# Kernel optimization log

Measured on AMD Instinct MI355X. Metric: run time of the kernel, lower is better.

The kernel has to match this reference:

```python
import math
import jax, jax.numpy as jnp
import numpy as np

NUM_HEADS = 16


def setup_inputs() -> dict:
    key = jax.random.key(0)
    ks = jax.random.split(key, 5)
    B, S, H = 2, 2048, 1024
    hidden_states = jax.random.normal(ks[0], (B, S, H), dtype=jnp.float32)
    # causal lower-triangular float mask [1, 1, S, S], as the module expects
    ltor_mask = jnp.tril(jnp.ones((S, S), dtype=jnp.float32))[None, None, :, :]
    # weights stored pre-transposed: y = x @ W + b (equivalent to torch Linear)
    W_qkv = jax.random.normal(ks[1], (H, 3 * H), dtype=jnp.float32) * (1.0 / math.sqrt(H))
    b_qkv = jnp.zeros((3 * H,), dtype=jnp.float32)
    W_dense = jax.random.normal(ks[2], (H, H), dtype=jnp.float32) * (1.0 / math.sqrt(H))
    b_dense = jnp.zeros((H,), dtype=jnp.float32)
    return {
        "hidden_states": hidden_states,
        "ltor_mask": ltor_mask,
        "W_qkv": W_qkv,
        "b_qkv": b_qkv,
        "W_dense": W_dense,
        "b_dense": b_dense,
    }


def reference(hidden_states, ltor_mask, W_qkv, b_qkv, W_dense, b_dense):
    B, S, H = hidden_states.shape
    nh = NUM_HEADS
    hd = H // nh

    # fused QKV projection: [B, S, 3H] -> split -> [B, nh, S, hd]
    qkv = hidden_states @ W_qkv + b_qkv
    q, k, v = jnp.split(qkv, 3, axis=-1)

    def to_heads(x):
        return x.reshape(B, S, nh, hd).transpose(0, 2, 1, 3)

    q, k, v = to_heads(q), to_heads(k), to_heads(v)

    # scaled dot-product scores [B, nh, S, S]
    scores = jnp.einsum("bhqd,bhkd->bhqk", q, k) / math.sqrt(hd)
    # mul/sub causal masking, exactly as the torch module does
    scores = scores * ltor_mask - 10000.0 * (1.0 - ltor_mask)
    probs = jax.nn.softmax(scores, axis=-1)
    # attention dropout omitted (eval mode / p=0.0)

    ctx = jnp.einsum("bhqk,bhkd->bhqd", probs, v)
    ctx = ctx.transpose(0, 2, 1, 3).reshape(B, S, H)

    out = ctx @ W_dense + b_dense
    # output dropout omitted (eval mode / p=0.0)
    return out
```

## Files before the change

kernel.cpp:

```cpp
#include <hip/hip_runtime.h>
#include <math.h>

#define BATCH 2
#define SEQ   2048
#define HID   1024
#define NHEAD 16
#define HDIM  64
#define MTOT  (BATCH * SEQ)
#define QKVN  (3 * HID)
#define HBUF  ((size_t)BATCH * NHEAD * SEQ * HDIM)

typedef _Float16 f16x8 __attribute__((ext_vector_type(8)));
typedef _Float16 f16x4 __attribute__((ext_vector_type(4)));
typedef float    f32x4 __attribute__((ext_vector_type(4)));

#define MFMA16(a, b, c) __builtin_amdgcn_mfma_f32_16x16x32_f16((a), (b), (c), 0, 0, 0)

#define GLDS16(gp, lp) __builtin_amdgcn_global_load_lds( \
    (const __attribute__((address_space(1))) void*)(gp), \
    (__attribute__((address_space(3))) void*)(lp), 16, 0, 0)

#if __has_builtin(__builtin_amdgcn_exp2f)
#define EXP2F(x) __builtin_amdgcn_exp2f(x)
#else
#define EXP2F(x) exp2f(x)
#endif

#define SCALE2 0.18033688011f
#define MASK2  -14426.950408f
#define BIAS2  -4.0f

__global__ __launch_bounds__(256) void prep_kernel(
    const float* __restrict__ hs, const float* __restrict__ Wqkv,
    const float* __restrict__ Wd, _Float16* __restrict__ A_h,
    _Float16* __restrict__ outQ, _Float16* __restrict__ outD)
{
    __shared__ _Float16 T[32][36];
    const int gid = blockIdx.x;
    const int tid = threadIdx.x;
    if (gid < 2048) {
        const int ci = gid * 256 + tid;
        const int m = ci >> 7, cc = ci & 127;
        const float* src = hs + (size_t)m * 1024 + cc * 8;
        f16x8 o;
#pragma unroll
        for (int j = 0; j < 8; ++j) o[j] = (_Float16)src[j];
        *(f16x8*)(A_h + (size_t)m * 1024 + cc * 8) = o;
        return;
    }
    const int tb = gid - 2048;
    const int bx = tb & 127, k0 = (tb >> 7) * 32;
    const float* in;
    _Float16* out;
    int N, n0;
    bool isQ;
    if (bx < 96) { in = Wqkv; out = outQ; N = QKVN; n0 = bx * 32; isQ = true; }
    else         { in = Wd;   out = outD; N = HID;  n0 = (bx - 96) * 32; isQ = false; }
    {
        const int r = tid >> 3, c4 = (tid & 7) * 4;
        float4 v = *(const float4*)(in + (size_t)(k0 + r) * N + n0 + c4);
        T[r][c4 + 0] = (_Float16)v.x;
        T[r][c4 + 1] = (_Float16)v.y;
        T[r][c4 + 2] = (_Float16)v.z;
        T[r][c4 + 3] = (_Float16)v.w;
    }
    __syncthreads();
    {
        const int nn = tid >> 3, k4 = (tid & 7) * 4;
        const int n = n0 + nn;
        f16x4 o;
        o[0] = T[k4 + 0][nn]; o[1] = T[k4 + 1][nn];
        o[2] = T[k4 + 2][nn]; o[3] = T[k4 + 3][nn];
        if (isQ) {
            *(f16x4*)(out + (size_t)n * 1024 + k0 + k4) = o;
        } else {
            const int pos = ((k4 >> 3) ^ (n & 3)), half = (k4 >> 2) & 1;
            *(f16x4*)(out + (size_t)n * 1024 + k0 + pos * 8 + half * 4) = o;
        }
    }
}

__global__ __launch_bounds__(512, 1) void qkv_gemm8(
    const _Float16* __restrict__ A, const _Float16* __restrict__ Bt,
    const float* __restrict__ bias, _Float16* __restrict__ base)
{
    __shared__ _Float16 SA[2][16384];
    __shared__ _Float16 SB[2][12288];
    const int tid = threadIdx.x;
    const int w = tid >> 6, l = tid & 63;
    const int a = l & 15, q4 = l >> 4, a7 = a & 7;
    const int xc = blockIdx.x & 7, loc = blockIdx.x >> 3;
    const int bx = (xc & 3) * 4 + (loc & 3);
    const int by = (xc >> 2) * 8 + (loc >> 2);
    const int m0 = by * 256, n0 = bx * 192;
    const int wm = (w >> 2) * 128, wn = (w & 3) * 48;

    const int csw = (((tid & 7) ^ ((tid >> 3) & 7)) << 3);
    const _Float16* gA0 = A  + (size_t)(m0 + (tid >> 3)) * 1024 + csw;
    const _Float16* gB0 = Bt + (size_t)(n0 + (tid >> 3)) * 1024 + csw;

    auto stage = [&](int kt, int sl) {
        const size_t ko = (size_t)kt * 64;
#pragma unroll
        for (int u = 0; u < 4; ++u)
            GLDS16(gA0 + (size_t)(u * 64) * 1024 + ko, &SA[sl][0] + u * 4096 + tid * 8);
#pragma unroll
        for (int u = 0; u < 3; ++u)
            GLDS16(gB0 + (size_t)(u * 64) * 1024 + ko, &SB[sl][0] + u * 4096 + tid * 8);
    };

    stage(0, 0); stage(1, 1);
    asm volatile("s_waitcnt vmcnt(7)" ::: "memory");
    __builtin_amdgcn_sched_barrier(0);
    __builtin_amdgcn_s_barrier();
    __builtin_amdgcn_sched_barrier(0);

    f32x4 acc[8][3];
#pragma unroll
    for (int i = 0; i < 8; ++i)
#pragma unroll
        for (int j = 0; j < 3; ++j) acc[i][j] = (f32x4){0.f, 0.f, 0.f, 0.f};

#define FRG(SP, row_, ks_) \
    (*(const f16x8*)&(SP)[(row_) * 64 + ((((ks_) * 4 + q4) ^ a7) << 3)])

    f16x8 aL[4][2], aH[4][2], bf[3][2];
    {
#pragma unroll
        for (int i = 0; i < 4; ++i) {
            aL[i][0] = FRG(SA[0], wm + i * 16 + a, 0);
            aL[i][1] = FRG(SA[0], wm + i * 16 + a, 1);
        }
#pragma unroll
        for (int j = 0; j < 2; ++j) {
            bf[j][0] = FRG(SB[0], wn + j * 16 + a, 0);
            bf[j][1] = FRG(SB[0], wn + j * 16 + a, 1);
        }
    }

    for (int t = 0; t < 16; ++t) {
        const int sl = t & 1, nsl = sl ^ 1;
        const _Float16* sA = &SA[sl][0];
        const _Float16* sB = &SB[sl][0];

        if (t >= 1 && t <= 14) stage(t + 1, nsl);

        __builtin_amdgcn_s_setprio(1);
#pragma unroll
        for (int i = 0; i < 4; ++i)
#pragma unroll
            for (int j = 0; j < 2; ++j) {
                acc[i][j] = MFMA16(aL[i][0], bf[j][0], acc[i][j]);
                acc[i][j] = MFMA16(aL[i][1], bf[j][1], acc[i][j]);
            }
        __builtin_amdgcn_s_setprio(0);

        bf[2][0] = FRG(sB, wn + 32 + a, 0);
        bf[2][1] = FRG(sB, wn + 32 + a, 1);
        __builtin_amdgcn_s_setprio(1);
#pragma unroll
        for (int i = 0; i < 4; ++i) {
            acc[i][2] = MFMA16(aL[i][0], bf[2][0], acc[i][2]);
            acc[i][2] = MFMA16(aL[i][1], bf[2][1], acc[i][2]);
        }
        __builtin_amdgcn_s_setprio(0);

#pragma unroll
        for (int i = 0; i < 4; ++i) {
            aH[i][0] = FRG(sA, wm + 64 + i * 16 + a, 0);
            aH[i][1] = FRG(sA, wm + 64 + i * 16 + a, 1);
        }
        __builtin_amdgcn_s_setprio(1);
#pragma unroll
        for (int i = 0; i < 4; ++i)
#pragma unroll
            for (int j = 0; j < 3; ++j) {
                acc[i + 4][j] = MFMA16(aH[i][0], bf[j][0], acc[i + 4][j]);
                acc[i + 4][j] = MFMA16(aH[i][1], bf[j][1], acc[i + 4][j]);
            }
        __builtin_amdgcn_s_setprio(0);

        if (t < 15) {
            asm volatile("s_waitcnt vmcnt(0)" ::: "memory");
            __builtin_amdgcn_sched_barrier(0);
            __builtin_amdgcn_s_barrier();
            __builtin_amdgcn_sched_barrier(0);
            const _Float16* nA = &SA[nsl][0];
            const _Float16* nB = &SB[nsl][0];
#pragma unroll
            for (int i = 0; i < 4; ++i) {
                aL[i][0] = FRG(nA, wm + i * 16 + a, 0);
                aL[i][1] = FRG(nA, wm + i * 16 + a, 1);
            }
#pragma unroll
            for (int j = 0; j < 2; ++j) {
                bf[j][0] = FRG(nB, wn + j * 16 + a, 0);
                bf[j][1] = FRG(nB, wn + j * 16 + a, 1);
            }
        }
    }
#undef FRG

#pragma unroll
    for (int j = 0; j < 3; ++j) {
        const int n = n0 + wn + 16 * j + a;
        const float bv = bias[n];
        const int tq = n >> 10, h = (n >> 6) & 15, d = n & 63;
#pragma unroll
        for (int i = 0; i < 8; ++i) {
            const int mb = m0 + wm + 16 * i + q4 * 4;
            const int bb = mb >> 11, sb = mb & 2047;
            if (tq == 2) {
                f16x4 ov;
#pragma unroll
                for (int r = 0; r < 4; ++r) ov[r] = (_Float16)(acc[i][j][r] + bv);
                const size_t off =
                    ((size_t)((bb * 16 + h) * 64 + d)) * 2048
                    + (sb & ~63)
                    + ((((sb >> 3) & 7) ^ (d & 7)) << 3) + (sb & 7);
                *(f16x4*)(base + 3 * HBUF + off) = ov;
            } else if (tq == 1) {
#pragma unroll
                for (int r = 0; r < 4; ++r) {
                    const int s = sb + r;
                    const _Float16 val = (_Float16)(acc[i][j][r] + bv);
                    const int dk = ((((d >> 3) ^ (s & 7)) & 7) << 3) | (d & 7);
                    base[HBUF + ((size_t)(bb * 16 + h) * 2048 + s) * 64 + dk] = val;
                }
            } else {
#pragma unroll
                for (int r = 0; r < 4; ++r) {
                    const _Float16 val = (_Float16)(acc[i][j][r] + bv);
                    base[((size_t)(bb * 16 + h) * 2048 + sb + r) * 64 + d] = val;
                }
            }
        }
    }
}

template<int EPI, int TM>
__global__ __launch_bounds__(256) void mfma_gemm(
    const _Float16* __restrict__ A, const _Float16* __restrict__ Bt,
    const float* __restrict__ bias, void* __restrict__ Cout,
    int M, int N, int K)
{
    __shared__ _Float16 As[TM * 32];
    __shared__ _Float16 Bs[128 * 32];
    constexpr int TI = TM / 32;
    constexpr int AR = TM / 4;

    const int tid = threadIdx.x;
    const int w = tid >> 6, l = tid & 63;
    const int a = l & 15, q4 = l >> 4;
    const int m0 = blockIdx.y * TM, n0 = blockIdx.x * 128;
    const int wm = (w >> 1) * (TM / 2), wn = (w & 1) * 64;

    f32x4 acc[TI][4];
#pragma unroll
    for (int i = 0; i < TI; ++i)
#pragma unroll
        for (int j = 0; j < 4; ++j) acc[i][j] = (f32x4){0.f, 0.f, 0.f, 0.f};

    const _Float16* gA = A + (size_t)(m0 + w * AR + (l >> 2)) * K + (l & 3) * 8;
    const _Float16* gB = Bt + (size_t)(n0 + w * 32 + (l >> 2)) * K + (l & 3) * 8;
    _Float16* sA = As + w * AR * 32;
    _Float16* sB = Bs + w * 1024;

    for (int k0 = 0; k0 < K; k0 += 32) {
#pragma unroll
        for (int u = 0; u < TM / 64; ++u)
            GLDS16(gA + (size_t)u * 16 * K + k0, sA + u * 512);
        GLDS16(gB + k0,          sB);
        GLDS16(gB + 16 * K + k0, sB + 512);
        __syncthreads();

        f16x8 af[TI], bf[4];
        const int pa = (q4 ^ (a & 3)) << 3;
#pragma unroll
        for (int i = 0; i < TI; ++i)
            af[i] = *(const f16x8*)&As[(wm + 16 * i + a) * 32 + pa];
#pragma unroll
        for (int j = 0; j < 4; ++j)
            bf[j] = *(const f16x8*)&Bs[(wn + 16 * j + a) * 32 + pa];
#pragma unroll
        for (int i = 0; i < TI; ++i)
#pragma unroll
            for (int j = 0; j < 4; ++j)
                acc[i][j] = MFMA16(af[i], bf[j], acc[i][j]);
        __syncthreads();
    }

    {
        float* C = (float*)Cout;
#pragma unroll
        for (int j = 0; j < 4; ++j) {
            const int n = n0 + wn + 16 * j + a;
            const float bv = bias[n];
#pragma unroll
            for (int i = 0; i < TI; ++i)
#pragma unroll
                for (int r = 0; r < 4; ++r) {
                    const int m = m0 + wm + 16 * i + q4 * 4 + r;
                    C[(size_t)m * N + n] = acc[i][j][r] + bv;
                }
        }
    }
}

__global__ __launch_bounds__(256, 2) void attn_mfma(
    const _Float16* __restrict__ qb, const _Float16* __restrict__ kb,
    const _Float16* __restrict__ vtb, _Float16* __restrict__ ctx)
{
    __shared__ _Float16 Ks[2][64 * 64];
    __shared__ _Float16 VT[2][64 * 64];
    __shared__ _Float16 Ps[4][16 * 64];

    const int bid = blockIdx.x;
    const int jj = bid >> 3;
    const int bhIdx = (bid & 7) * 4 + (jj >> 4);
    const int p = jj & 15;
    const int b = bhIdx >> 4, h = bhIdx & 15;
    const int tid = threadIdx.x;
    const int w = tid >> 6, l = tid & 63;
    const int a = l & 15, q4 = l >> 4, a7 = a & 7;
    const size_t bh  = ((size_t)b * NHEAD + h) * SEQ;
    const size_t bhd = ((size_t)b * NHEAD + h) * 64;

    const int qHi = (31 - p) * 64 + w * 16;
    const int qLo = p * 64 + w * 16;
    const int ntiles = 32 - p;

    f16x8 qfh[2], qfl[2];
    {
        const _Float16* qp = qb + (bh + qHi + a) * 64;
        qfh[0] = *(const f16x8*)(qp + q4 * 8);
        qfh[1] = *(const f16x8*)(qp + 32 + q4 * 8);
        const _Float16* ql = qb + (bh + qLo + a) * 64;
        qfl[0] = *(const f16x8*)(ql + q4 * 8);
        qfl[1] = *(const f16x8*)(ql + 32 + q4 * 8);
    }

    f32x4 Oh[4], Ol[4];
#pragma unroll
    for (int c = 0; c < 4; ++c) {
        Oh[c] = (f32x4){0.f, 0.f, 0.f, 0.f};
        Ol[c] = (f32x4){0.f, 0.f, 0.f, 0.f};
    }
    float lh = 0.f, ll = 0.f;

    const _Float16* kg = kb + (bh + w * 16) * 64 + l * 8;
    const int vrow = w * 16 + (l >> 3);
    const _Float16* vg = vtb + (bhd + vrow) * 2048 + (l & 7) * 8;
    _Float16* pbuf = &Ps[w][0];
    const int p0 = (q4 ^ a7) << 3;

    auto stage = [&](int t, int buf) {
        _Float16* ksl = &Ks[buf][0] + w * 1024 + l * 8;
        const _Float16* kt = kg + (size_t)t * 4096;
        GLDS16(kt,       ksl);
        GLDS16(kt + 512, ksl + 512);
        _Float16* vtl = &VT[buf][0] + vrow * 64 + (l & 7) * 8;
        GLDS16(vg + t * 64,            vtl);
        GLDS16(vg + t * 64 + 8 * 2048, vtl + 512);
    };

    stage(0, 0);

    for (int t = 0; t < ntiles; ++t) {
        __syncthreads();
        if (t + 1 < ntiles) stage(t + 1, (t + 1) & 1);

        const _Float16* ksb  = &Ks[t & 1][0];
        const _Float16* vbuf = &VT[t & 1][0];
        const int kt0 = t * 64;
        const bool doLo = (t <= p);

        f32x4 sh[4], sl[4];
        __builtin_amdgcn_s_setprio(1);
#pragma unroll
        for (int n0 = 0; n0 < 4; ++n0) {
            f16x8 kf0 = *(const f16x8*)&ksb[(n0 * 16 + a) * 64 + p0];
            f16x8 kf1 = *(const f16x8*)&ksb[(n0 * 16 + a) * 64 + (p0 ^ 32)];
            f32x4 c = (f32x4){0.f, 0.f, 0.f, 0.f};
            c = MFMA16(kf0, qfh[0], c);
            c = MFMA16(kf1, qfh[1], c);
            sh[n0] = c;
            if (doLo) {
                f32x4 d = (f32x4){0.f, 0.f, 0.f, 0.f};
                d = MFMA16(kf0, qfl[0], d);
                d = MFMA16(kf1, qfl[1], d);
                sl[n0] = d;
            }
        }
        __builtin_amdgcn_s_setprio(0);

        auto half_step = [&](f32x4 st[4], float& lrun, f32x4* O,
                             const bool maskT, const int qbase) {
            if (maskT) {
#pragma unroll
                for (int n0 = 0; n0 < 4; ++n0)
#pragma unroll
                    for (int r = 0; r < 4; ++r) {
                        const int kgl = kt0 + n0 * 16 + q4 * 4 + r;
                        st[n0][r] = (kgl > qbase + a) ? MASK2
                                                      : fmaf(st[n0][r], SCALE2, BIAS2);
                    }
            } else {
#pragma unroll
                for (int n0 = 0; n0 < 4; ++n0)
#pragma unroll
                    for (int r = 0; r < 4; ++r)
                        st[n0][r] = fmaf(st[n0][r], SCALE2, BIAS2);
            }
            float ls = 0.f;
#pragma unroll
            for (int n0 = 0; n0 < 4; ++n0)
#pragma unroll
                for (int r = 0; r < 4; ++r) {
                    const float pe = EXP2F(st[n0][r]);
                    st[n0][r] = pe;
                    ls += pe;
                }
            lrun += ls;
#pragma unroll
            for (int n0 = 0; n0 < 4; ++n0) {
                f16x4 pk;
#pragma unroll
                for (int r = 0; r < 4; ++r) pk[r] = (_Float16)st[n0][r];
                const int pos = (2 * n0 + (q4 >> 1)) ^ a7;
                *(f16x4*)&pbuf[a * 64 + pos * 8 + ((q4 & 1) << 2)] = pk;
            }
            f16x8 pf0 = *(const f16x8*)&pbuf[a * 64 + p0];
            f16x8 pf1 = *(const f16x8*)&pbuf[a * 64 + (p0 ^ 32)];
            __builtin_amdgcn_s_setprio(1);
#pragma unroll
            for (int c = 0; c < 4; ++c) {
                f16x8 vf0 = *(const f16x8*)&vbuf[(c * 16 + a) * 64 + p0];
                f16x8 vf1 = *(const f16x8*)&vbuf[(c * 16 + a) * 64 + (p0 ^ 32)];
                O[c] = MFMA16(vf0, pf0, O[c]);
                O[c] = MFMA16(vf1, pf1, O[c]);
            }
            __builtin_amdgcn_s_setprio(0);
        };

        half_step(sh, lh, Oh, t == 31 - p, qHi);
        if (doLo) half_step(sl, ll, Ol, t == p, qLo);
    }

    auto finish = [&](float lrun, const f32x4* O, const int qbase) {
        float lt = lrun;
        lt += __shfl_xor(lt, 16);
        lt += __shfl_xor(lt, 32);
        const float inv = 1.0f / lt;
        const size_t row = (size_t)b * SEQ + qbase + a;
#pragma unroll
        for (int c = 0; c < 4; ++c) {
            const int d0 = c * 16 + q4 * 4;
            const int kcol = h * 64 + (d0 & ~31)
                           + ((((d0 >> 3) & 3) ^ (a & 3)) << 3) + (d0 & 7);
            f16x4 ov;
#pragma unroll
            for (int r = 0; r < 4; ++r) ov[r] = (_Float16)(O[c][r] * inv);
            *(f16x4*)(ctx + row * HID + kcol) = ov;
        }
    };
    finish(lh, Oh, qHi);
    finish(ll, Ol, qLo);
}

extern "C" void kernel_launch(void* const* d_in, const int* in_sizes, int n_in,
                              void* d_out, int out_size, void* d_ws, size_t ws_size,
                              hipStream_t stream) {
    const float* hs   = (const float*)d_in[0];
    const float* Wqkv = (const float*)d_in[2];
    const float* bqkv = (const float*)d_in[3];
    const float* Wd   = (const float*)d_in[4];
    const float* bd   = (const float*)d_in[5];

    _Float16* A_h   = (_Float16*)d_ws;
    _Float16* WqkvT = A_h + (size_t)MTOT * HID;
    _Float16* WdT   = WqkvT + (size_t)QKVN * HID;
    _Float16* qbuf  = WdT + (size_t)HID * HID;
    _Float16* ctxb  = qbuf + 4 * HBUF;

    prep_kernel<<<6144, 256, 0, stream>>>(hs, Wqkv, Wd, A_h, WqkvT, WdT);

    qkv_gemm8<<<256, 512, 0, stream>>>(A_h, WqkvT, bqkv, qbuf);

    attn_mfma<<<512, 256, 0, stream>>>(
        qbuf, qbuf + HBUF, qbuf + 3 * HBUF, ctxb);

    mfma_gemm<1, 64><<<dim3(HID / 128, MTOT / 64), 256, 0, stream>>>(
        ctxb, WdT, bd, d_out, MTOT, HID, HID);
}
```

Measured before the change: 185.4 us.

## Split attention KV tiles across two wave groups and merge partial outputs

Doubles the attention block to 512 threads. Two groups of four waves each process alternating KV tiles for the same query rows, using separate double-buffered K/V shared memory, then combine their partial O and row sums through shared memory before normalising. This works because the softmax uses a fixed offset instead of a running max, so partial sums can simply be added. It aims to shorten the serial KV loop per block and raise wave-level parallelism on the MI355X's 256 CUs, at the cost of more shared memory, an extra reduction step, and possible occupancy limits with launch_bounds(512,2).

Measured after the change: 190.4 us. 1.03x slower.

```diff
diff --git a/kernel.cpp b/kernel.cpp
--- a/kernel.cpp
+++ b/kernel.cpp
@@ -307,13 +307,13 @@
     }
 }
 
-__global__ __launch_bounds__(256, 2) void attn_mfma(
+__global__ __launch_bounds__(512, 2) void attn_mfma(
     const _Float16* __restrict__ qb, const _Float16* __restrict__ kb,
     const _Float16* __restrict__ vtb, _Float16* __restrict__ ctx)
 {
-    __shared__ _Float16 Ks[2][64 * 64];
-    __shared__ _Float16 VT[2][64 * 64];
-    __shared__ _Float16 Ps[4][16 * 64];
+    __shared__ _Float16 Ks[2][2][64 * 64];
+    __shared__ _Float16 VT[2][2][64 * 64];
+    __shared__ _Float16 Ps[8][16 * 64];
 
     const int bid = blockIdx.x;
     const int jj = bid >> 3;
@@ -322,13 +322,15 @@
     const int b = bhIdx >> 4, h = bhIdx & 15;
     const int tid = threadIdx.x;
     const int w = tid >> 6, l = tid & 63;
+    const int sgrp = w >> 2, w4 = w & 3;
     const int a = l & 15, q4 = l >> 4, a7 = a & 7;
     const size_t bh  = ((size_t)b * NHEAD + h) * SEQ;
     const size_t bhd = ((size_t)b * NHEAD + h) * 64;
 
-    const int qHi = (31 - p) * 64 + w * 16;
-    const int qLo = p * 64 + w * 16;
+    const int qHi = (31 - p) * 64 + w4 * 16;
+    const int qLo = p * 64 + w4 * 16;
     const int ntiles = 32 - p;
+    const int NIT = (ntiles + 1) >> 1;
 
     f16x8 qfh[2], qfl[2];
     {
@@ -348,124 +350,156 @@
     }
     float lh = 0.f, ll = 0.f;
 
-    const _Float16* kg = kb + (bh + w * 16) * 64 + l * 8;
-    const int vrow = w * 16 + (l >> 3);
+    const _Float16* kg = kb + (bh + w4 * 16) * 64 + l * 8;
+    const int vrow = w4 * 16 + (l >> 3);
     const _Float16* vg = vtb + (bhd + vrow) * 2048 + (l & 7) * 8;
     _Float16* pbuf = &Ps[w][0];
     const int p0 = (q4 ^ a7) << 3;
 
     auto stage = [&](int t, int buf) {
-        _Float16* ksl = &Ks[buf][0] + w * 1024 + l * 8;
+        _Float16* ksl = &Ks[sgrp][buf][0] + w4 * 1024 + l * 8;
         const _Float16* kt = kg + (size_t)t * 4096;
         GLDS16(kt,       ksl);
         GLDS16(kt + 512, ksl + 512);
-        _Float16* vtl = &VT[buf][0] + vrow * 64 + (l & 7) * 8;
+        _Float16* vtl = &VT[sgrp][buf][0] + vrow * 64 + (l & 7) * 8;
         GLDS16(vg + t * 64,            vtl);
         GLDS16(vg + t * 64 + 8 * 2048, vtl + 512);
     };
 
-    stage(0, 0);
-
-    for (int t = 0; t < ntiles; ++t) {
+    stage(sgrp, 0);
+
+    for (int it = 0; it < NIT; ++it) {
         __syncthreads();
-        if (t + 1 < ntiles) stage(t + 1, (t + 1) & 1);
-
-        const _Float16* ksb  = &Ks[t & 1][0];
-        const _Float16* vbuf = &VT[t & 1][0];
-        const int kt0 = t * 64;
-        const bool doLo = (t <= p);
-
-        f32x4 sh[4], sl[4];
-        __builtin_amdgcn_s_setprio(1);
-#pragma unroll
-        for (int n0 = 0; n0 < 4; ++n0) {
-            f16x8 kf0 = *(const f16x8*)&ksb[(n0 * 16 + a) * 64 + p0];
-            f16x8 kf1 = *(const f16x8*)&ksb[(n0 * 16 + a) * 64 + (p0 ^ 32)];
-            f32x4 c = (f32x4){0.f, 0.f, 0.f, 0.f};
-            c = MFMA16(kf0, qfh[0], c);
-            c = MFMA16(kf1, qfh[1], c);
-            sh[n0] = c;
-            if (doLo) {
-                f32x4 d = (f32x4){0.f, 0.f, 0.f, 0.f};
-                d = MFMA16(kf0, qfl[0], d);
-                d = MFMA16(kf1, qfl[1], d);
-                sl[n0] = d;
-            }
-        }
-        __builtin_amdgcn_s_setprio(0);
-
-        auto half_step = [&](f32x4 st[4], float& lrun, f32x4* O,
-                             const bool maskT, const int qbase) {
-            if (maskT) {
+        const int t = sgrp + 2 * it;
+        const int buf = it & 1;
+        if (t + 2 < ntiles) stage(t + 2, buf ^ 1);
+        if (t < ntiles) {
+            const _Float16* ksb  = &Ks[sgrp][buf][0];
+            const _Float16* vbuf = &VT[sgrp][buf][0];
+            const int kt0 = t * 64;
+            const bool doLo = (t <= p);
+
+            f32x4 sh[4], sl[4];
+            __builtin_amdgcn_s_setprio(1);
+#pragma unroll
+            for (int n0 = 0; n0 < 4; ++n0) {
+                f16x8 kf0 = *(const f16x8*)&ksb[(n0 * 16 + a) * 64 + p0];
+                f16x8 kf1 = *(const f16x8*)&ksb[(n0 * 16 + a) * 64 + (p0 ^ 32)];
+                f32x4 c = (f32x4){0.f, 0.f, 0.f, 0.f};
+                c = MFMA16(kf0, qfh[0], c);
+                c = MFMA16(kf1, qfh[1], c);
+                sh[n0] = c;
+                if (doLo) {
+                    f32x4 d = (f32x4){0.f, 0.f, 0.f, 0.f};
+                    d = MFMA16(kf0, qfl[0], d);
+                    d = MFMA16(kf1, qfl[1], d);
+                    sl[n0] = d;
+                }
+            }
+            __builtin_amdgcn_s_setprio(0);
+
+            auto half_step = [&](f32x4 st[4], float& lrun, f32x4* O,
+                                 const bool maskT, const int qbase) {
+                if (maskT) {
+#pragma unroll
+                    for (int n0 = 0; n0 < 4; ++n0)
+#pragma unroll
+                        for (int r = 0; r < 4; ++r) {
+                            const int kgl = kt0 + n0 * 16 + q4 * 4 + r;
+                            st[n0][r] = (kgl > qbase + a) ? MASK2
+                                                          : fmaf(st[n0][r], SCALE2, BIAS2);
+                        }
+                } else {
+#pragma unroll
+                    for (int n0 = 0; n0 < 4; ++n0)
+#pragma unroll
+                        for (int r = 0; r < 4; ++r)
+                            st[n0][r] = fmaf(st[n0][r], SCALE2, BIAS2);
+                }
+                float ls = 0.f;
 #pragma unroll
                 for (int n0 = 0; n0 < 4; ++n0)
 #pragma unroll
                     for (int r = 0; r < 4; ++r) {
-                        const int kgl = kt0 + n0 * 16 + q4 * 4 + r;
-                        st[n0][r] = (kgl > qbase + a) ? MASK2
-                                                      : fmaf(st[n0][r], SCALE2, BIAS2);
+                        const float pe = EXP2F(st[n0][r]);
+                        st[n0][r] = pe;
+                        ls += pe;
                     }
-            } else {
-#pragma unroll
-                for (int n0 = 0; n0 < 4; ++n0)
-#pragma unroll
-                    for (int r = 0; r < 4; ++r)
-                        st[n0][r] = fmaf(st[n0][r], SCALE2, BIAS2);
-            }
-            float ls = 0.f;
-#pragma unroll
-            for (int n0 = 0; n0 < 4; ++n0)
-#pragma unroll
-                for (int r = 0; r < 4; ++r) {
-                    const float pe = EXP2F(st[n0][r]);
-                    st[n0][r] = pe;
-                    ls += pe;
-                }
-            lrun += ls;
-#pragma unroll
-            for (int n0 = 0; n0 < 4; ++n0) {
-                f16x4 pk;
-#pragma unroll
-                for (int r = 0; r < 4; ++r) pk[r] = (_Float16)st[n0][r];
-                const int pos = (2 * n0 + (q4 >> 1)) ^ a7;
-                *(f16x4*)&pbuf[a * 64 + pos * 8 + ((q4 & 1) << 2)] = pk;
-            }
-            f16x8 pf0 = *(const f16x8*)&pbuf[a * 64 + p0];
-            f16x8 pf1 = *(const f16x8*)&pbuf[a * 64 + (p0 ^ 32)];
-            __builtin_amdgcn_s_setprio(1);
+                lrun += ls;
+#pragma unroll
+                for (int n0 = 0; n0 < 4; ++n0) {
+                    f16x4 pk;
+#pragma unroll
+                    for (int r = 0; r < 4; ++r) pk[r] = (_Float16)st[n0][r];
+                    const int pos = (2 * n0 + (q4 >> 1)) ^ a7;
+                    *(f16x4*)&pbuf[a * 64 + pos * 8 + ((q4 & 1) << 2)] = pk;
+                }
+                f16x8 pf0 = *(const f16x8*)&pbuf[a * 64 + p0];
+                f16x8 pf1 = *(const f16x8*)&pbuf[a * 64 + (p0 ^ 32)];
+                __builtin_amdgcn_s_setprio(1);
+#pragma unroll
+                for (int c = 0; c < 4; ++c) {
+                    f16x8 vf0 = *(const f16x8*)&vbuf[(c * 16 + a) * 64 + p0];
+                    f16x8 vf1 = *(const f16x8*)&vbuf[(c * 16 + a) * 64 + (p0 ^ 32)];
+                    O[c] = MFMA16(vf0, pf0, O[c]);
+                    O[c] = MFMA16(vf1, pf1, O[c]);
+                }
+                __builtin_amdgcn_s_setprio(0);
+            };
+
+            half_step(sh, lh, Oh, t == 31 - p, qHi);
+            if (doLo) half_step(sl, ll, Ol, t == p, qLo);
+        }
+    }
+
+    __syncthreads();
+    float* cO = (float*)&Ks[0][0][0];
+    float* cL = (float*)&VT[0][0][0];
+    if (sgrp == 1) {
+        const int cbase = w4 * 2048;
+#pragma unroll
+        for (int c = 0; c < 4; ++c)
+#pragma unroll
+            for (int r = 0; r < 4; ++r) {
+                cO[cbase + (c * 4 + r) * 64 + l]        = Oh[c][r];
+                cO[cbase + (16 + c * 4 + r) * 64 + l]   = Ol[c][r];
+            }
+        cL[w4 * 128 + l]      = lh;
+        cL[w4 * 128 + 64 + l] = ll;
+    }
+    __syncthreads();
+    if (sgrp == 0) {
+        const int cbase = w4 * 2048;
+#pragma unroll
+        for (int c = 0; c < 4; ++c)
+#pragma unroll
+            for (int r = 0; r < 4; ++r) {
+                Oh[c][r] += cO[cbase + (c * 4 + r) * 64 + l];
+                Ol[c][r] += cO[cbase + (16 + c * 4 + r) * 64 + l];
+            }
+        lh += cL[w4 * 128 + l];
+        ll += cL[w4 * 128 + 64 + l];
+
+        auto finish = [&](float lrun, const f32x4* O, const int qbase) {
+            float lt = lrun;
+            lt += __shfl_xor(lt, 16);
+            lt += __shfl_xor(lt, 32);
+            const float inv = 1.0f / lt;
+            const size_t row = (size_t)b * SEQ + qbase + a;
 #pragma unroll
             for (int c = 0; c < 4; ++c) {
-                f16x8 vf0 = *(const f16x8*)&vbuf[(c * 16 + a) * 64 + p0];
-                f16x8 vf1 = *(const f16x8*)&vbuf[(c * 16 + a) * 64 + (p0 ^ 32)];
-                O[c] = MFMA16(vf0, pf0, O[c]);
-                O[c] = MFMA16(vf1, pf1, O[c]);
-            }
-            __builtin_amdgcn_s_setprio(0);
+                const int d0 = c * 16 + q4 * 4;
+                const int kcol = h * 64 + (d0 & ~31)
+                               + ((((d0 >> 3) & 3) ^ (a & 3)) << 3) + (d0 & 7);
+                f16x4 ov;
+#pragma unroll
+                for (int r = 0; r < 4; ++r) ov[r] = (_Float16)(O[c][r] * inv);
+                *(f16x4*)(ctx + row * HID + kcol) = ov;
+            }
         };
-
-        half_step(sh, lh, Oh, t == 31 - p, qHi);
-        if (doLo) half_step(sl, ll, Ol, t == p, qLo);
-    }
-
-    auto finish = [&](float lrun, const f32x4* O, const int qbase) {
-        float lt = lrun;
-        lt += __shfl_xor(lt, 16);
-        lt += __shfl_xor(lt, 32);
-        const float inv = 1.0f / lt;
-        const size_t row = (size_t)b * SEQ + qbase + a;
-#pragma unroll
-        for (int c = 0; c < 4; ++c) {
-            const int d0 = c * 16 + q4 * 4;
-            const int kcol = h * 64 + (d0 & ~31)
-                           + ((((d0 >> 3) & 3) ^ (a & 3)) << 3) + (d0 & 7);
-            f16x4 ov;
-#pragma unroll
-            for (int r = 0; r < 4; ++r) ov[r] = (_Float16)(O[c][r] * inv);
-            *(f16x4*)(ctx + row * HID + kcol) = ov;
-        }
-    };
-    finish(lh, Oh, qHi);
-    finish(ll, Ol, qLo);
+        finish(lh, Oh, qHi);
+        finish(ll, Ol, qLo);
+    }
 }
 
 extern "C" void kernel_launch(void* const* d_in, const int* in_sizes, int n_in,
@@ -487,7 +521,7 @@
 
     qkv_gemm8<<<256, 512, 0, stream>>>(A_h, WqkvT, bqkv, qbuf);
 
-    attn_mfma<<<512, 256, 0, stream>>>(
+    attn_mfma<<<512, 512, 0, stream>>>(
         qbuf, qbuf + HBUF, qbuf + 3 * HBUF, ctxb);
 
     mfma_gemm<1, 64><<<dim3(HID / 128, MTOT / 64), 256, 0, stream>>>(
```

## Load K/V attention fragments directly from global memory instead of LDS staging

Applied to the files above, without the earlier changes.

The attention kernel no longer double-buffers K and V tiles in shared memory through async global-to-LDS copies with a barrier each iteration. Each wave now loads its own K and V MFMA fragments straight from global memory into registers. To make that possible, the QKV projection epilogue now writes K and transposed V in plain unswizzled layouts. The intent is to remove per-tile barriers and LDS traffic, at the cost of four-fold redundant global/L2 loads per block and less latency hiding. The occupancy hint of 2 blocks per CU is also dropped from launch_bounds.

Result: slower. 260.8 us (+40.7%).

```diff
diff --git a/kernel.cpp b/kernel.cpp
--- a/kernel.cpp
+++ b/kernel.cpp
@@ -214,24 +214,14 @@
                 f16x4 ov;
 #pragma unroll
                 for (int r = 0; r < 4; ++r) ov[r] = (_Float16)(acc[i][j][r] + bv);
-                const size_t off =
-                    ((size_t)((bb * 16 + h) * 64 + d)) * 2048
-                    + (sb & ~63)
-                    + ((((sb >> 3) & 7) ^ (d & 7)) << 3) + (sb & 7);
-                *(f16x4*)(base + 3 * HBUF + off) = ov;
-            } else if (tq == 1) {
-#pragma unroll
-                for (int r = 0; r < 4; ++r) {
-                    const int s = sb + r;
-                    const _Float16 val = (_Float16)(acc[i][j][r] + bv);
-                    const int dk = ((((d >> 3) ^ (s & 7)) & 7) << 3) | (d & 7);
-                    base[HBUF + ((size_t)(bb * 16 + h) * 2048 + s) * 64 + dk] = val;
-                }
+                *(f16x4*)(base + 3 * HBUF
+                          + ((size_t)((bb * 16 + h) * 64 + d)) * 2048 + sb) = ov;
             } else {
 #pragma unroll
                 for (int r = 0; r < 4; ++r) {
                     const _Float16 val = (_Float16)(acc[i][j][r] + bv);
-                    base[((size_t)(bb * 16 + h) * 2048 + sb + r) * 64 + d] = val;
+                    base[(size_t)tq * HBUF
+                         + ((size_t)(bb * 16 + h) * 2048 + sb + r) * 64 + d] = val;
                 }
             }
         }
@@ -307,12 +297,10 @@
     }
 }
 
-__global__ __launch_bounds__(256, 2) void attn_mfma(
+__global__ __launch_bounds__(256) void attn_mfma(
     const _Float16* __restrict__ qb, const _Float16* __restrict__ kb,
     const _Float16* __restrict__ vtb, _Float16* __restrict__ ctx)
 {
-    __shared__ _Float16 Ks[2][64 * 64];
-    __shared__ _Float16 VT[2][64 * 64];
     __shared__ _Float16 Ps[4][16 * 64];
 
     const int bid = blockIdx.x;
@@ -348,47 +336,42 @@
     }
     float lh = 0.f, ll = 0.f;
 
-    const _Float16* kg = kb + (bh + w * 16) * 64 + l * 8;
-    const int vrow = w * 16 + (l >> 3);
-    const _Float16* vg = vtb + (bhd + vrow) * 2048 + (l & 7) * 8;
+    const _Float16* kfp = kb + (bh + a) * 64 + q4 * 8;
+    const _Float16* vfp = vtb + (bhd + a) * 2048 + q4 * 8;
     _Float16* pbuf = &Ps[w][0];
     const int p0 = (q4 ^ a7) << 3;
 
-    auto stage = [&](int t, int buf) {
-        _Float16* ksl = &Ks[buf][0] + w * 1024 + l * 8;
-        const _Float16* kt = kg + (size_t)t * 4096;
-        GLDS16(kt,       ksl);
-        GLDS16(kt + 512, ksl + 512);
-        _Float16* vtl = &VT[buf][0] + vrow * 64 + (l & 7) * 8;
-        GLDS16(vg + t * 64,            vtl);
-        GLDS16(vg + t * 64 + 8 * 2048, vtl + 512);
-    };
-
-    stage(0, 0);
-
     for (int t = 0; t < ntiles; ++t) {
-        __syncthreads();
-        if (t + 1 < ntiles) stage(t + 1, (t + 1) & 1);
-
-        const _Float16* ksb  = &Ks[t & 1][0];
-        const _Float16* vbuf = &VT[t & 1][0];
         const int kt0 = t * 64;
         const bool doLo = (t <= p);
 
+        f16x8 kf[4][2];
+#pragma unroll
+        for (int n0 = 0; n0 < 4; ++n0) {
+            const _Float16* kr = kfp + (size_t)(kt0 + n0 * 16) * 64;
+            kf[n0][0] = *(const f16x8*)(kr);
+            kf[n0][1] = *(const f16x8*)(kr + 32);
+        }
+        f16x8 vf[4][2];
+#pragma unroll
+        for (int c = 0; c < 4; ++c) {
+            const _Float16* vr = vfp + (size_t)(c * 16) * 2048 + kt0;
+            vf[c][0] = *(const f16x8*)(vr);
+            vf[c][1] = *(const f16x8*)(vr + 32);
+        }
+
         f32x4 sh[4], sl[4];
         __builtin_amdgcn_s_setprio(1);
 #pragma unroll
         for (int n0 = 0; n0 < 4; ++n0) {
-            f16x8 kf0 = *(const f16x8*)&ksb[(n0 * 16 + a) * 64 + p0];
-            f16x8 kf1 = *(const f16x8*)&ksb[(n0 * 16 + a) * 64 + (p0 ^ 32)];
             f32x4 c = (f32x4){0.f, 0.f, 0.f, 0.f};
-            c = MFMA16(kf0, qfh[0], c);
-            c = MFMA16(kf1, qfh[1], c);
+            c = MFMA16(kf[n0][0], qfh[0], c);
+            c = MFMA16(kf[n0][1], qfh[1], c);
             sh[n0] = c;
             if (doLo) {
                 f32x4 d = (f32x4){0.f, 0.f, 0.f, 0.f};
-                d = MFMA16(kf0, qfl[0], d);
-                d = MFMA16(kf1, qfl[1], d);
+                d = MFMA16(kf[n0][0], qfl[0], d);
+                d = MFMA16(kf[n0][1], qfl[1], d);
                 sl[n0] = d;
             }
         }
@@ -435,10 +418,8 @@
             __builtin_amdgcn_s_setprio(1);
 #pragma unroll
             for (int c = 0; c < 4; ++c) {
-                f16x8 vf0 = *(const f16x8*)&vbuf[(c * 16 + a) * 64 + p0];
-                f16x8 vf1 = *(const f16x8*)&vbuf[(c * 16 + a) * 64 + (p0 ^ 32)];
-                O[c] = MFMA16(vf0, pf0, O[c]);
-                O[c] = MFMA16(vf1, pf1, O[c]);
+                O[c] = MFMA16(vf[c][0], pf0, O[c]);
+                O[c] = MFMA16(vf[c][1], pf1, O[c]);
             }
             __builtin_amdgcn_s_setprio(0);
         };
```

## Replace dense output GEMM with double-buffered 128x128 pipelined kernel

Applied to the files above, without the earlier changes.

Replaces the generic single-buffered 64x128 dense GEMM with a 512-thread 128x128-tile kernel. It stages K-slices of 64 into double-buffered LDS with an XOR swizzle applied at load time, overlapping global-to-LDS copies with MFMA work, and uses a grouped block mapping. The ctx and WdT layouts drop their old pre-swizzle since the new kernel swizzles on staging. The attention kernel now loads V fragments early in each tile instead of inside the PV step, which raises register pressure.

After: 180.0 us. -2.9%, faster.

```diff
diff --git a/kernel.cpp b/kernel.cpp
--- a/kernel.cpp
+++ b/kernel.cpp
@@ -53,9 +53,8 @@
     const float* in;
     _Float16* out;
     int N, n0;
-    bool isQ;
-    if (bx < 96) { in = Wqkv; out = outQ; N = QKVN; n0 = bx * 32; isQ = true; }
-    else         { in = Wd;   out = outD; N = HID;  n0 = (bx - 96) * 32; isQ = false; }
+    if (bx < 96) { in = Wqkv; out = outQ; N = QKVN; n0 = bx * 32; }
+    else         { in = Wd;   out = outD; N = HID;  n0 = (bx - 96) * 32; }
     {
         const int r = tid >> 3, c4 = (tid & 7) * 4;
         float4 v = *(const float4*)(in + (size_t)(k0 + r) * N + n0 + c4);
@@ -71,12 +70,7 @@
         f16x4 o;
         o[0] = T[k4 + 0][nn]; o[1] = T[k4 + 1][nn];
         o[2] = T[k4 + 2][nn]; o[3] = T[k4 + 3][nn];
-        if (isQ) {
-            *(f16x4*)(out + (size_t)n * 1024 + k0 + k4) = o;
-        } else {
-            const int pos = ((k4 >> 3) ^ (n & 3)), half = (k4 >> 2) & 1;
-            *(f16x4*)(out + (size_t)n * 1024 + k0 + pos * 8 + half * 4) = o;
-        }
+        *(f16x4*)(out + (size_t)n * 1024 + k0 + k4) = o;
     }
 }
 
@@ -238,72 +232,96 @@
     }
 }
 
-template<int EPI, int TM>
-__global__ __launch_bounds__(256) void mfma_gemm(
+__global__ __launch_bounds__(512, 1) void dense_gemm8(
     const _Float16* __restrict__ A, const _Float16* __restrict__ Bt,
-    const float* __restrict__ bias, void* __restrict__ Cout,
-    int M, int N, int K)
+    const float* __restrict__ bias, float* __restrict__ C)
 {
-    __shared__ _Float16 As[TM * 32];
-    __shared__ _Float16 Bs[128 * 32];
-    constexpr int TI = TM / 32;
-    constexpr int AR = TM / 4;
-
+    __shared__ _Float16 SA[2][8192];
+    __shared__ _Float16 SB[2][8192];
     const int tid = threadIdx.x;
     const int w = tid >> 6, l = tid & 63;
-    const int a = l & 15, q4 = l >> 4;
-    const int m0 = blockIdx.y * TM, n0 = blockIdx.x * 128;
-    const int wm = (w >> 1) * (TM / 2), wn = (w & 1) * 64;
-
-    f32x4 acc[TI][4];
-#pragma unroll
-    for (int i = 0; i < TI; ++i)
-#pragma unroll
-        for (int j = 0; j < 4; ++j) acc[i][j] = (f32x4){0.f, 0.f, 0.f, 0.f};
-
-    const _Float16* gA = A + (size_t)(m0 + w * AR + (l >> 2)) * K + (l & 3) * 8;
-    const _Float16* gB = Bt + (size_t)(n0 + w * 32 + (l >> 2)) * K + (l & 3) * 8;
-    _Float16* sA = As + w * AR * 32;
-    _Float16* sB = Bs + w * 1024;
-
-    for (int k0 = 0; k0 < K; k0 += 32) {
-#pragma unroll
-        for (int u = 0; u < TM / 64; ++u)
-            GLDS16(gA + (size_t)u * 16 * K + k0, sA + u * 512);
-        GLDS16(gB + k0,          sB);
-        GLDS16(gB + 16 * K + k0, sB + 512);
-        __syncthreads();
-
-        f16x8 af[TI], bf[4];
-        const int pa = (q4 ^ (a & 3)) << 3;
-#pragma unroll
-        for (int i = 0; i < TI; ++i)
-            af[i] = *(const f16x8*)&As[(wm + 16 * i + a) * 32 + pa];
-#pragma unroll
-        for (int j = 0; j < 4; ++j)
-            bf[j] = *(const f16x8*)&Bs[(wn + 16 * j + a) * 32 + pa];
-#pragma unroll
-        for (int i = 0; i < TI; ++i)
-#pragma unroll
-            for (int j = 0; j < 4; ++j)
-                acc[i][j] = MFMA16(af[i], bf[j], acc[i][j]);
-        __syncthreads();
-    }
-
-    {
-        float* C = (float*)Cout;
-#pragma unroll
-        for (int j = 0; j < 4; ++j) {
-            const int n = n0 + wn + 16 * j + a;
-            const float bv = bias[n];
-#pragma unroll
-            for (int i = 0; i < TI; ++i)
-#pragma unroll
-                for (int r = 0; r < 4; ++r) {
-                    const int m = m0 + wm + 16 * i + q4 * 4 + r;
-                    C[(size_t)m * N + n] = acc[i][j][r] + bv;
-                }
-        }
+    const int a = l & 15, q4 = l >> 4, a7 = a & 7;
+    const int xc = blockIdx.x & 7, loc = blockIdx.x >> 3;
+    const int bx = loc >> 2;
+    const int by = xc * 4 + (loc & 3);
+    const int m0 = by * 128, n0 = bx * 128;
+    const int wm = (w >> 2) * 64, wn = (w & 3) * 32;
+
+    const int csw = (((tid & 7) ^ ((tid >> 3) & 7)) << 3);
+    const _Float16* gA0 = A  + (size_t)(m0 + (tid >> 3)) * 1024 + csw;
+    const _Float16* gB0 = Bt + (size_t)(n0 + (tid >> 3)) * 1024 + csw;
+
+    auto stage = [&](int kt, int sl) {
+        const size_t ko = (size_t)kt * 64;
+        GLDS16(gA0 + ko,                     &SA[sl][0] + tid * 8);
+        GLDS16(gA0 + (size_t)64 * 1024 + ko, &SA[sl][0] + 4096 + tid * 8);
+        GLDS16(gB0 + ko,                     &SB[sl][0] + tid * 8);
+        GLDS16(gB0 + (size_t)64 * 1024 + ko, &SB[sl][0] + 4096 + tid * 8);
+    };
+
+    stage(0, 0); stage(1, 1);
+    asm volatile("s_waitcnt vmcnt(4)" ::: "memory");
+    __builtin_amdgcn_sched_barrier(0);
+    __builtin_amdgcn_s_barrier();
+    __builtin_amdgcn_sched_barrier(0);
+
+    f32x4 acc[4][2];
+#pragma unroll
+    for (int i = 0; i < 4; ++i)
+#pragma unroll
+        for (int j = 0; j < 2; ++j) acc[i][j] = (f32x4){0.f, 0.f, 0.f, 0.f};
+
+#define FRG(SP, row_, ks_) \
+    (*(const f16x8*)&(SP)[(row_) * 64 + ((((ks_) * 4 + q4) ^ a7) << 3)])
+
+    for (int t = 0; t < 16; ++t) {
+        const int sl = t & 1, nsl = sl ^ 1;
+        const _Float16* sA = &SA[sl][0];
+        const _Float16* sB = &SB[sl][0];
+
+        if (t >= 1 && t <= 14) stage(t + 1, nsl);
+
+        f16x8 af[4][2], bfr[2][2];
+#pragma unroll
+        for (int j = 0; j < 2; ++j) {
+            bfr[j][0] = FRG(sB, wn + j * 16 + a, 0);
+            bfr[j][1] = FRG(sB, wn + j * 16 + a, 1);
+        }
+#pragma unroll
+        for (int i = 0; i < 4; ++i) {
+            af[i][0] = FRG(sA, wm + i * 16 + a, 0);
+            af[i][1] = FRG(sA, wm + i * 16 + a, 1);
+        }
+        __builtin_amdgcn_s_setprio(1);
+#pragma unroll
+        for (int i = 0; i < 4; ++i)
+#pragma unroll
+            for (int j = 0; j < 2; ++j) {
+                acc[i][j] = MFMA16(af[i][0], bfr[j][0], acc[i][j]);
+                acc[i][j] = MFMA16(af[i][1], bfr[j][1], acc[i][j]);
+            }
+        __builtin_amdgcn_s_setprio(0);
+
+        if (t < 15) {
+            asm volatile("s_waitcnt vmcnt(0)" ::: "memory");
+            __builtin_amdgcn_sched_barrier(0);
+            __builtin_amdgcn_s_barrier();
+            __builtin_amdgcn_sched_barrier(0);
+        }
+    }
+#undef FRG
+
+#pragma unroll
+    for (int j = 0; j < 2; ++j) {
+        const int n = n0 + wn + 16 * j + a;
+        const float bv = bias[n];
+#pragma unroll
+        for (int i = 0; i < 4; ++i)
+#pragma unroll
+            for (int r = 0; r < 4; ++r) {
+                const int m = m0 + wm + 16 * i + q4 * 4 + r;
+                C[(size_t)m * 1024 + n] = acc[i][j][r] + bv;
+            }
     }
 }
 
@@ -374,6 +392,13 @@
         const _Float16* vbuf = &VT[t & 1][0];
         const int kt0 = t * 64;
         const bool doLo = (t <= p);
+
+        f16x8 vf[4][2];
+#pragma unroll
+        for (int c = 0; c < 4; ++c) {
+            vf[c][0] = *(const f16x8*)&vbuf[(c * 16 + a) * 64 + p0];
+            vf[c][1] = *(const f16x8*)&vbuf[(c * 16 + a) * 64 + (p0 ^ 32)];
+        }
 
         f32x4 sh[4], sl[4];
         __builtin_amdgcn_s_setprio(1);
@@ -435,10 +460,8 @@
             __builtin_amdgcn_s_setprio(1);
 #pragma unroll
             for (int c = 0; c < 4; ++c) {
-                f16x8 vf0 = *(const f16x8*)&vbuf[(c * 16 + a) * 64 + p0];
-                f16x8 vf1 = *(const f16x8*)&vbuf[(c * 16 + a) * 64 + (p0 ^ 32)];
-                O[c] = MFMA16(vf0, pf0, O[c]);
-                O[c] = MFMA16(vf1, pf1, O[c]);
+                O[c] = MFMA16(vf[c][0], pf0, O[c]);
+                O[c] = MFMA16(vf[c][1], pf1, O[c]);
             }
             __builtin_amdgcn_s_setprio(0);
         };
@@ -455,9 +478,7 @@
         const size_t row = (size_t)b * SEQ + qbase + a;
 #pragma unroll
         for (int c = 0; c < 4; ++c) {
-            const int d0 = c * 16 + q4 * 4;
-            const int kcol = h * 64 + (d0 & ~31)
-                           + ((((d0 >> 3) & 3) ^ (a & 3)) << 3) + (d0 & 7);
+            const int kcol = h * 64 + c * 16 + q4 * 4;
             f16x4 ov;
 #pragma unroll
             for (int r = 0; r < 4; ++r) ov[r] = (_Float16)(O[c][r] * inv);
@@ -490,6 +511,5 @@
     attn_mfma<<<512, 256, 0, stream>>>(
         qbuf, qbuf + HBUF, qbuf + 3 * HBUF, ctxb);
 
-    mfma_gemm<1, 64><<<dim3(HID / 128, MTOT / 64), 256, 0, stream>>>(
-        ctxb, WdT, bd, d_out, MTOT, HID, HID);
+    dense_gemm8<<<256, 512, 0, stream>>>(ctxb, WdT, bd, (float*)d_out);
 }
```
